# Performance work log

Measured on AMD Instinct MI355X. Metric: run time of the kernel, lower is better.

The kernel has to match this reference:

```python
import jax, jax.numpy as jnp
import numpy as np

HEAD_SIZE = 128
NEG_INF = -1000000000.0

def setup_inputs() -> dict:
    key = jax.random.key(0)
    k1, k2, k3, k4 = jax.random.split(key, 4)
    B, T, C = 8, 2048, 1024
    x = jax.random.normal(k1, (B, T, C), dtype=jnp.float32)
    Wq = jax.random.normal(k2, (C, HEAD_SIZE), dtype=jnp.float32) * (1.0 / np.sqrt(C))
    Wk = jax.random.normal(k3, (C, HEAD_SIZE), dtype=jnp.float32) * (1.0 / np.sqrt(C))
    Wv = jax.random.normal(k4, (C, HEAD_SIZE), dtype=jnp.float32) * (1.0 / np.sqrt(C))
    return {"x": x, "Wq": Wq, "Wk": Wk, "Wv": Wv}

def reference(x, Wq, Wk, Wv):
    # x: [B, T, C]; projections: [B, T, H]
    T = x.shape[1]
    q = jnp.einsum('btc,ch->bth', x, Wq)
    k = jnp.einsum('btc,ch->bth', x, Wk)
    v = jnp.einsum('btc,ch->bth', x, Wv)
    scale = 1.0 / jnp.sqrt(jnp.float32(HEAD_SIZE))
    wei = jnp.einsum('bth,bsh->bts', q, k) * scale  # [B, T, T]
    causal = jnp.tril(jnp.ones((T, T), dtype=bool))
    wei = jnp.where(causal, wei, NEG_INF)
    wei = jax.nn.softmax(wei, axis=-1)
    # dropout is identity (deterministic=True)
    out = jnp.einsum('bts,bsh->bth', wei, v)  # [B, T, H]
    return out
```

## Files before the change

kernel.cpp:

```cpp
#include <hip/hip_runtime.h>
#include <hip/hip_bf16.h>
#include <stdint.h>

#define B_ 8
#define T_ 2048
#define C_ 1024
#define H_ 128
#define BT (B_*T_)
#define SCALE 0.08838834764831845f
#define CH 4
#define SLOTS_PB 140

typedef __attribute__((ext_vector_type(8))) short bf16x8;
typedef __attribute__((ext_vector_type(4))) float f32x4;

__device__ __forceinline__ ushort f2bf(float f) {
  union { float f; uint32_t u; } un; un.f = f;
  return (ushort)((un.u + 0x7fffu + ((un.u >> 16) & 1u)) >> 16);
}
__device__ __forceinline__ float bf2f(ushort h) {
  union { uint32_t u; float f; } un; un.u = ((uint32_t)h) << 16;
  return un.f;
}
__device__ __forceinline__ void gload16(const void* g, void* l) {
  __builtin_amdgcn_global_load_lds(
      (const __attribute__((address_space(1))) void*)g,
      (__attribute__((address_space(3))) void*)l, 16, 0, 0);
}

__global__ __launch_bounds__(256) void wtrans_kernel(
    const float* __restrict__ Wq, const float* __restrict__ Wk,
    const float* __restrict__ Wv, ushort* __restrict__ wt)
{
  const int tt = blockIdx.x * 256 + threadIdx.x;
  const int n = tt >> 6;
  const int k0 = (tt & 63) << 4;
  const float* W = (n < 128) ? Wq : (n < 256 ? Wk : Wv);
  const int h = n & 127;
  ushort tmp[16];
  #pragma unroll
  for (int j = 0; j < 16; ++j)
    tmp[j] = f2bf(W[(size_t)(k0 + j) * H_ + h]);
  *reinterpret_cast<bf16x8*>(&wt[(size_t)n * C_ + k0]) =
      *reinterpret_cast<bf16x8*>(&tmp[0]);
  *reinterpret_cast<bf16x8*>(&wt[(size_t)n * C_ + k0 + 8]) =
      *reinterpret_cast<bf16x8*>(&tmp[8]);
}

__global__ __launch_bounds__(256, 3) void proj_kernel(
    const float* __restrict__ x, const ushort* __restrict__ wt,
    ushort* __restrict__ qh, ushort* __restrict__ kh, ushort* __restrict__ vt)
{
  __shared__ __align__(16) ushort As[64][64];
  __shared__ __align__(16) ushort Bs[128][64];
  const int tid  = threadIdx.x;
  const int lane = tid & 63, wave = tid >> 6;
  const int l15  = lane & 15, l4 = lane >> 4;
  const int o  = (blockIdx.x & 7) * 96 + (blockIdx.x >> 3);
  const int mb = o / 3, nb = o - mb * 3;
  const int m0 = mb * 64, n0 = nb * 128;
  const int wr = wave >> 1, wc = wave & 1;

  f32x4 acc[2][4];
  #pragma unroll
  for (int i = 0; i < 2; ++i)
    #pragma unroll
    for (int j = 0; j < 4; ++j) acc[i][j] = f32x4{0.f, 0.f, 0.f, 0.f};

  for (int k0 = 0; k0 < C_; k0 += 64) {
    __syncthreads();
    #pragma unroll
    for (int j = 0; j < 4; ++j) {
      const int seg = wave * 4 + j;
      const int r = seg * 8 + (lane >> 3);
      const int c8g = (lane & 7) ^ (r & 7);
      gload16(&wt[(size_t)(n0 + r) * C_ + k0 + c8g * 8], &Bs[seg * 8][0]);
    }
    float4 av[4];
    #pragma unroll
    for (int it = 0; it < 4; ++it) {
      const int f4 = it * 256 + tid;
      const int r = f4 >> 4, c4 = f4 & 15;
      av[it] = *reinterpret_cast<const float4*>(
          &x[(size_t)(m0 + r) * C_ + k0 + 4 * c4]);
    }
    #pragma unroll
    for (int it = 0; it < 4; ++it) {
      const int f4 = it * 256 + tid;
      const int r = f4 >> 4, c4 = f4 & 15;
      ushort4 pk;
      pk.x = f2bf(av[it].x); pk.y = f2bf(av[it].y);
      pk.z = f2bf(av[it].z); pk.w = f2bf(av[it].w);
      const int ch = (c4 >> 1) ^ (r & 7);
      *reinterpret_cast<ushort4*>(&As[r][ch * 8 + (c4 & 1) * 4]) = pk;
    }
    __syncthreads();

    bf16x8 a[2][2], b[4][2];
    #pragma unroll
    for (int mi = 0; mi < 2; ++mi)
      #pragma unroll
      for (int kc = 0; kc < 2; ++kc) {
        const int row = wr * 32 + mi * 16 + l15;
        const int ch = (kc * 4 + l4) ^ (row & 7);
        a[mi][kc] = *reinterpret_cast<const bf16x8*>(&As[row][ch * 8]);
      }
    #pragma unroll
    for (int ni = 0; ni < 4; ++ni)
      #pragma unroll
      for (int kc = 0; kc < 2; ++kc) {
        const int row = wc * 64 + ni * 16 + l15;
        const int ch = (kc * 4 + l4) ^ (row & 7);
        b[ni][kc] = *reinterpret_cast<const bf16x8*>(&Bs[row][ch * 8]);
      }

    __builtin_amdgcn_s_setprio(1);
    if (nb != 2) {
      #pragma unroll
      for (int mi = 0; mi < 2; ++mi)
        #pragma unroll
        for (int ni = 0; ni < 4; ++ni)
          #pragma unroll
          for (int kc = 0; kc < 2; ++kc)
            acc[mi][ni] = __builtin_amdgcn_mfma_f32_16x16x32_bf16(
                a[mi][kc], b[ni][kc], acc[mi][ni], 0, 0, 0);
    } else {
      #pragma unroll
      for (int mi = 0; mi < 2; ++mi)
        #pragma unroll
        for (int ni = 0; ni < 4; ++ni)
          #pragma unroll
          for (int kc = 0; kc < 2; ++kc)
            acc[mi][ni] = __builtin_amdgcn_mfma_f32_16x16x32_bf16(
                b[ni][kc], a[mi][kc], acc[mi][ni], 0, 0, 0);
    }
    __builtin_amdgcn_s_setprio(0);
  }

  if (nb != 2) {
    ushort* dst = (nb == 0) ? qh : kh;
    const float mul = (nb == 0) ? SCALE : 1.0f;
    #pragma unroll
    for (int mi = 0; mi < 2; ++mi)
      #pragma unroll
      for (int ni = 0; ni < 4; ++ni)
        #pragma unroll
        for (int reg = 0; reg < 4; ++reg) {
          const int row = m0 + wr * 32 + mi * 16 + l4 * 4 + reg;
          const int col = wc * 64 + ni * 16 + l15;
          dst[(size_t)row * H_ + col] = f2bf(acc[mi][ni][reg] * mul);
        }
  } else {
    #pragma unroll
    for (int mi = 0; mi < 2; ++mi)
      #pragma unroll
      for (int ni = 0; ni < 4; ++ni)
        #pragma unroll
        for (int reg = 0; reg < 4; ++reg) {
          const int h = wc * 64 + ni * 16 + l4 * 4 + reg;
          const int gr = m0 + wr * 32 + mi * 16 + l15;
          const int b = gr >> 11, t = gr & 2047;
          vt[((size_t)b * H_ + h) * T_ + t] = f2bf(acc[mi][ni][reg]);
        }
  }
}

__global__ __launch_bounds__(256) void attn_kernel(
    const ushort* __restrict__ qh, const ushort* __restrict__ kh,
    const ushort* __restrict__ vt, ushort* __restrict__ pO,
    float* __restrict__ pm, float* __restrict__ pl, float* __restrict__ out)
{
  __shared__ __align__(16) ushort Ks[64][128];
  __shared__ __align__(16) ushort Vs[128][64];
  __shared__ __align__(16) ushort Ps[4][16][64];
  const int tid  = threadIdx.x;
  const int lane = tid & 63, wave = tid >> 6;
  const int l15  = lane & 15, l4 = lane >> 4;
  const int o = (blockIdx.x & 7) * 144 + (blockIdx.x >> 3);
  const int b = o / 144;
  const int u = o - b * 144;
  int qi, ci, nchunk, u2 = 0;
  if (u < 4) { qi = u; ci = 0; nchunk = 1; }
  else {
    u2 = u - 4;
    int rem = u2, g = 1;
    while (rem >= 4 * (g + 1)) { rem -= 4 * (g + 1); ++g; }
    nchunk = g + 1;
    qi = 4 * g + rem / nchunk;
    ci = rem - (rem / nchunk) * nchunk;
  }
  const int q0 = qi * 64;
  const int kt0 = ci * CH;
  const int kt1 = min(qi + 1, kt0 + CH);
  const size_t mbase = (size_t)b * T_ + q0;
  const int swz = l15 & 7;

  bf16x8 qa[4];
  {
    const ushort* qrow = &qh[(mbase + wave * 16 + l15) * H_];
    #pragma unroll
    for (int kc = 0; kc < 4; ++kc)
      qa[kc] = *reinterpret_cast<const bf16x8*>(&qrow[kc * 32 + l4 * 8]);
  }

  f32x4 o_[8];
  #pragma unroll
  for (int i = 0; i < 8; ++i) o_[i] = f32x4{0.f, 0.f, 0.f, 0.f};
  float mrow[4] = {-1e9f, -1e9f, -1e9f, -1e9f};
  float lrow[4] = {0.f, 0.f, 0.f, 0.f};

  for (int kt = kt0; kt < kt1; ++kt) {
    const int kv0 = kt * 64;
    __syncthreads();
    #pragma unroll
    for (int j = 0; j < 4; ++j) {
      const int r0 = wave * 16 + j * 4;
      const int r = r0 + (lane >> 4);
      const int c8 = lane & 15;
      const int c8g = (c8 & 8) | ((c8 & 7) ^ (r & 7));
      gload16(&kh[((size_t)b * T_ + kv0 + r) * H_ + c8g * 8], &Ks[r0][0]);
    }
    #pragma unroll
    for (int j = 0; j < 4; ++j) {
      const int r0 = wave * 32 + j * 8;
      const int r = r0 + (lane >> 3);
      const int c8g = (lane & 7) ^ (r & 7);
      gload16(&vt[((size_t)b * H_ + r) * T_ + kv0 + c8g * 8], &Vs[r0][0]);
    }
    __syncthreads();

    f32x4 s[4];
    __builtin_amdgcn_s_setprio(1);
    #pragma unroll
    for (int ct = 0; ct < 4; ++ct) {
      s[ct] = f32x4{0.f, 0.f, 0.f, 0.f};
      #pragma unroll
      for (int kc = 0; kc < 4; ++kc) {
        const int chunk = ((kc * 4 + l4) & 7) ^ swz;
        bf16x8 kb = *reinterpret_cast<const bf16x8*>(
            &Ks[ct * 16 + l15][(((kc * 4 + l4) & 8) | chunk) * 8]);
        s[ct] = __builtin_amdgcn_mfma_f32_16x16x32_bf16(qa[kc], kb, s[ct], 0, 0, 0);
      }
    }
    __builtin_amdgcn_s_setprio(0);

    const bool diag = (kv0 == q0);
    float sv[4][4];
    #pragma unroll
    for (int ct = 0; ct < 4; ++ct)
      #pragma unroll
      for (int reg = 0; reg < 4; ++reg) {
        float v = s[ct][reg];
        if (diag) {
          const int sg = kv0 + ct * 16 + l15;
          const int rg = q0 + wave * 16 + l4 * 4 + reg;
          if (sg > rg) v = -1e9f;
        }
        sv[ct][reg] = v;
      }
    float mnew[4], alpha[4], ls[4];
    #pragma unroll
    for (int reg = 0; reg < 4; ++reg) {
      float m = fmaxf(fmaxf(sv[0][reg], sv[1][reg]), fmaxf(sv[2][reg], sv[3][reg]));
      #pragma unroll
      for (int msk = 1; msk < 16; msk <<= 1) m = fmaxf(m, __shfl_xor(m, msk));
      mnew[reg]  = fmaxf(mrow[reg], m);
      alpha[reg] = __expf(mrow[reg] - mnew[reg]);
      ls[reg] = 0.f;
    }
    #pragma unroll
    for (int ct = 0; ct < 4; ++ct)
      #pragma unroll
      for (int reg = 0; reg < 4; ++reg) {
        const float p = __expf(sv[ct][reg] - mnew[reg]);
        ls[reg] += p;
        const int prow = l4 * 4 + reg;
        Ps[wave][prow][(ct * 16 + l15) ^ ((prow & 7) * 8)] = f2bf(p);
      }
    #pragma unroll
    for (int reg = 0; reg < 4; ++reg) {
      float t = ls[reg];
      #pragma unroll
      for (int msk = 1; msk < 16; msk <<= 1) t += __shfl_xor(t, msk);
      lrow[reg] = lrow[reg] * alpha[reg] + t;
      mrow[reg] = mnew[reg];
    }
    #pragma unroll
    for (int ct = 0; ct < 8; ++ct)
      #pragma unroll
      for (int reg = 0; reg < 4; ++reg) o_[ct][reg] *= alpha[reg];
    bf16x8 pa[2];
    #pragma unroll
    for (int kc = 0; kc < 2; ++kc)
      pa[kc] = *reinterpret_cast<const bf16x8*>(
          &Ps[wave][l15][((kc * 4 + l4) ^ swz) * 8]);
    __builtin_amdgcn_s_setprio(1);
    #pragma unroll
    for (int ct = 0; ct < 8; ++ct) {
      #pragma unroll
      for (int kc = 0; kc < 2; ++kc) {
        bf16x8 vb = *reinterpret_cast<const bf16x8*>(
            &Vs[ct * 16 + l15][((kc * 4 + l4) ^ swz) * 8]);
        o_[ct] = __builtin_amdgcn_mfma_f32_16x16x32_bf16(pa[kc], vb, o_[ct], 0, 0, 0);
      }
    }
    __builtin_amdgcn_s_setprio(0);
  }

  if (nchunk == 1) {
    #pragma unroll
    for (int ct = 0; ct < 8; ++ct)
      #pragma unroll
      for (int reg = 0; reg < 4; ++reg) {
        const size_t row = mbase + wave * 16 + l4 * 4 + reg;
        out[row * H_ + ct * 16 + l15] = o_[ct][reg] / lrow[reg];
      }
  } else {
    const size_t slot = (size_t)b * SLOTS_PB + u2;
    ushort* po = pO + slot * 64 * 128;
    #pragma unroll
    for (int ct = 0; ct < 8; ++ct)
      #pragma unroll
      for (int reg = 0; reg < 4; ++reg) {
        const int row = wave * 16 + l4 * 4 + reg;
        po[(size_t)row * 128 + ct * 16 + l15] = f2bf(o_[ct][reg]);
      }
    #pragma unroll
    for (int reg = 0; reg < 4; ++reg) {
      if (l15 == 0) {
        const int row = wave * 16 + l4 * 4 + reg;
        pm[slot * 64 + row] = mrow[reg];
        pl[slot * 64 + row] = lrow[reg];
      }
    }
  }
}

__global__ __launch_bounds__(256) void combine_kernel(
    const ushort* __restrict__ pO, const float* __restrict__ pm,
    const float* __restrict__ pl, float* __restrict__ out)
{
  const int o = blockIdx.x;
  const int b = o / 28, qi = 4 + o % 28;
  const int G = qi >> 2;
  const int nc = G + 1;
  const int tid = threadIdx.x;
  const int row = tid >> 2, cg = tid & 3;
  const size_t slotbase =
      (size_t)b * SLOTS_PB + 2 * (G - 1) * (G + 2) + (qi & 3) * (G + 1);

  float M = -1e30f;
  for (int ci = 0; ci < nc; ++ci)
    M = fmaxf(M, pm[(slotbase + ci) * 64 + row]);

  float L = 0.f;
  float acc[32];
  #pragma unroll
  for (int j = 0; j < 32; ++j) acc[j] = 0.f;
  for (int ci = 0; ci < nc; ++ci) {
    const float e = __expf(pm[(slotbase + ci) * 64 + row] - M);
    L += pl[(slotbase + ci) * 64 + row] * e;
    const ushort* src = pO + (slotbase + ci) * 8192 + (size_t)row * 128 + cg * 32;
    #pragma unroll
    for (int j4 = 0; j4 < 4; ++j4) {
      bf16x8 v = *reinterpret_cast<const bf16x8*>(&src[j4 * 8]);
      #pragma unroll
      for (int j = 0; j < 8; ++j)
        acc[j4 * 8 + j] += e * bf2f((ushort)v[j]);
    }
  }
  const float inv = 1.f / L;
  float* dst = out + ((size_t)b * T_ + qi * 64 + row) * H_ + cg * 32;
  #pragma unroll
  for (int j4 = 0; j4 < 8; ++j4) {
    float4 w;
    w.x = acc[j4 * 4 + 0] * inv; w.y = acc[j4 * 4 + 1] * inv;
    w.z = acc[j4 * 4 + 2] * inv; w.w = acc[j4 * 4 + 3] * inv;
    *reinterpret_cast<float4*>(&dst[j4 * 4]) = w;
  }
}

extern "C" void kernel_launch(void* const* d_in, const int* in_sizes, int n_in,
                              void* d_out, int out_size, void* d_ws, size_t ws_size,
                              hipStream_t stream) {
  const float* x  = (const float*)d_in[0];
  const float* Wq = (const float*)d_in[1];
  const float* Wk = (const float*)d_in[2];
  const float* Wv = (const float*)d_in[3];
  float* out = (float*)d_out;
  ushort* qh = (ushort*)d_ws;
  ushort* kh = qh + (size_t)BT * H_;
  ushort* vt = kh + (size_t)BT * H_;
  ushort* wt = vt + (size_t)B_ * H_ * T_;
  ushort* pO = wt + (size_t)384 * C_;
  float*  pm = (float*)(pO + (size_t)B_ * SLOTS_PB * 64 * 128);
  float*  pl = pm + (size_t)B_ * SLOTS_PB * 64;
  wtrans_kernel<<<96, 256, 0, stream>>>(Wq, Wk, Wv, wt);
  proj_kernel<<<768, 256, 0, stream>>>(x, wt, qh, kh, vt);
  attn_kernel<<<1152, 256, 0, stream>>>(qh, kh, vt, pO, pm, pl, out);
  combine_kernel<<<224, 256, 0, stream>>>(pO, pm, pl, out);
}
```

Baseline: 79.89 us.

## Prefetch next tile into registers in projection GEMM and attention loops

In the projection GEMM, the next x tile's float4 loads are issued before the current tile is computed, and converted and stored to LDS at the start of the next iteration. In the attention kernel, the direct global-to-LDS K/V loads are replaced by register prefetch of the next K/V tile during compute, written to LDS after a barrier at the end of each iteration. This is meant to hide global memory latency behind MFMA work, at the cost of extra VGPRs (kreg/vreg, av) that may reduce occupancy.

```diff
diff --git a/kernel.cpp b/kernel.cpp
--- a/kernel.cpp
+++ b/kernel.cpp
@@ -67,16 +67,8 @@
     #pragma unroll
     for (int j = 0; j < 4; ++j) acc[i][j] = f32x4{0.f, 0.f, 0.f, 0.f};
 
-  for (int k0 = 0; k0 < C_; k0 += 64) {
-    __syncthreads();
-    #pragma unroll
-    for (int j = 0; j < 4; ++j) {
-      const int seg = wave * 4 + j;
-      const int r = seg * 8 + (lane >> 3);
-      const int c8g = (lane & 7) ^ (r & 7);
-      gload16(&wt[(size_t)(n0 + r) * C_ + k0 + c8g * 8], &Bs[seg * 8][0]);
-    }
-    float4 av[4];
+  float4 av[4];
+  auto a_issue = [&](int k0) {
     #pragma unroll
     for (int it = 0; it < 4; ++it) {
       const int f4 = it * 256 + tid;
@@ -84,6 +76,8 @@
       av[it] = *reinterpret_cast<const float4*>(
           &x[(size_t)(m0 + r) * C_ + k0 + 4 * c4]);
     }
+  };
+  auto a_write = [&]() {
     #pragma unroll
     for (int it = 0; it < 4; ++it) {
       const int f4 = it * 256 + tid;
@@ -94,6 +88,21 @@
       const int ch = (c4 >> 1) ^ (r & 7);
       *reinterpret_cast<ushort4*>(&As[r][ch * 8 + (c4 & 1) * 4]) = pk;
     }
+  };
+
+  a_issue(0);
+  for (int t = 0; t < 16; ++t) {
+    const int k0 = t * 64;
+    __syncthreads();
+    #pragma unroll
+    for (int j = 0; j < 4; ++j) {
+      const int seg = wave * 4 + j;
+      const int r = seg * 8 + (lane >> 3);
+      const int c8g = (lane & 7) ^ (r & 7);
+      gload16(&wt[(size_t)(n0 + r) * C_ + k0 + c8g * 8], &Bs[seg * 8][0]);
+    }
+    a_write();
+    if (t < 15) a_issue(k0 + 64);
     __syncthreads();
 
     bf16x8 a[2][2], b[4][2];
@@ -203,31 +212,53 @@
       qa[kc] = *reinterpret_cast<const bf16x8*>(&qrow[kc * 32 + l4 * 8]);
   }
 
+  bf16x8 kreg[4], vreg[4];
+  auto kv_issue = [&](int kv0) {
+    #pragma unroll
+    for (int j = 0; j < 4; ++j) {
+      const int i = j * 256 + tid;
+      const int r = i >> 4, c8 = i & 15;
+      kreg[j] = *reinterpret_cast<const bf16x8*>(
+          &kh[((size_t)b * T_ + kv0 + r) * H_ + c8 * 8]);
+    }
+    #pragma unroll
+    for (int j = 0; j < 4; ++j) {
+      const int i = j * 256 + tid;
+      const int r = i >> 3, c8 = i & 7;
+      vreg[j] = *reinterpret_cast<const bf16x8*>(
+          &vt[((size_t)b * H_ + r) * T_ + kv0 + c8 * 8]);
+    }
+  };
+  auto kv_write = [&]() {
+    #pragma unroll
+    for (int j = 0; j < 4; ++j) {
+      const int i = j * 256 + tid;
+      const int r = i >> 4, c8 = i & 15;
+      const int c8s = (c8 & 7) ^ (r & 7);
+      *reinterpret_cast<bf16x8*>(&Ks[r][((c8 & 8) | c8s) * 8]) = kreg[j];
+    }
+    #pragma unroll
+    for (int j = 0; j < 4; ++j) {
+      const int i = j * 256 + tid;
+      const int r = i >> 3, c8 = i & 7;
+      const int c8s = c8 ^ (r & 7);
+      *reinterpret_cast<bf16x8*>(&Vs[r][c8s * 8]) = vreg[j];
+    }
+  };
+
   f32x4 o_[8];
   #pragma unroll
   for (int i = 0; i < 8; ++i) o_[i] = f32x4{0.f, 0.f, 0.f, 0.f};
   float mrow[4] = {-1e9f, -1e9f, -1e9f, -1e9f};
   float lrow[4] = {0.f, 0.f, 0.f, 0.f};
 
+  kv_issue(kt0 * 64);
+  kv_write();
+
   for (int kt = kt0; kt < kt1; ++kt) {
     const int kv0 = kt * 64;
     __syncthreads();
-    #pragma unroll
-    for (int j = 0; j < 4; ++j) {
-      const int r0 = wave * 16 + j * 4;
-      const int r = r0 + (lane >> 4);
-      const int c8 = lane & 15;
-      const int c8g = (c8 & 8) | ((c8 & 7) ^ (r & 7));
-      gload16(&kh[((size_t)b * T_ + kv0 + r) * H_ + c8g * 8], &Ks[r0][0]);
-    }
-    #pragma unroll
-    for (int j = 0; j < 4; ++j) {
-      const int r0 = wave * 32 + j * 8;
-      const int r = r0 + (lane >> 3);
-      const int c8g = (lane & 7) ^ (r & 7);
-      gload16(&vt[((size_t)b * H_ + r) * T_ + kv0 + c8g * 8], &Vs[r0][0]);
-    }
-    __syncthreads();
+    if (kt + 1 < kt1) kv_issue((kt + 1) * 64);
 
     f32x4 s[4];
     __builtin_amdgcn_s_setprio(1);
@@ -305,6 +336,9 @@
       }
     }
     __builtin_amdgcn_s_setprio(0);
+
+    __syncthreads();
+    if (kt + 1 < kt1) kv_write();
   }
 
   if (nchunk == 1) {
```

New measurement: 80.56 us. Within noise of the previous version (+0.8%).

## Double-buffer projection GEMM and load weights directly into registers

Applied to the files above, without the earlier changes.

Rewrites the projection kernel's K loop as a software pipeline. The A tile is double-buffered in LDS, and the next step's x and weight loads are issued before the current step's MFMAs. Weight fragments now go from global memory straight into registers, so the Bs shared tile and its LDS round trip are gone. This should hide global-load latency and leave one barrier per step, but it raises register pressure and makes weight reads uncoalesced, which may conflict with the occupancy target of 3 set in the launch bounds.

```diff
diff --git a/kernel.cpp b/kernel.cpp
--- a/kernel.cpp
+++ b/kernel.cpp
@@ -51,8 +51,8 @@
     const float* __restrict__ x, const ushort* __restrict__ wt,
     ushort* __restrict__ qh, ushort* __restrict__ kh, ushort* __restrict__ vt)
 {
-  __shared__ __align__(16) ushort As[64][64];
-  __shared__ __align__(16) ushort Bs[128][64];
+  __shared__ __align__(16) ushort As0[64][64];
+  __shared__ __align__(16) ushort As1[64][64];
   const int tid  = threadIdx.x;
   const int lane = tid & 63, wave = tid >> 6;
   const int l15  = lane & 15, l4 = lane >> 4;
@@ -67,74 +67,89 @@
     #pragma unroll
     for (int j = 0; j < 4; ++j) acc[i][j] = f32x4{0.f, 0.f, 0.f, 0.f};
 
-  for (int k0 = 0; k0 < C_; k0 += 64) {
-    __syncthreads();
-    #pragma unroll
-    for (int j = 0; j < 4; ++j) {
-      const int seg = wave * 4 + j;
-      const int r = seg * 8 + (lane >> 3);
-      const int c8g = (lane & 7) ^ (r & 7);
-      gload16(&wt[(size_t)(n0 + r) * C_ + k0 + c8g * 8], &Bs[seg * 8][0]);
-    }
-    float4 av[4];
-    #pragma unroll
-    for (int it = 0; it < 4; ++it) {
-      const int f4 = it * 256 + tid;
-      const int r = f4 >> 4, c4 = f4 & 15;
-      av[it] = *reinterpret_cast<const float4*>(
-          &x[(size_t)(m0 + r) * C_ + k0 + 4 * c4]);
-    }
-    #pragma unroll
-    for (int it = 0; it < 4; ++it) {
-      const int f4 = it * 256 + tid;
-      const int r = f4 >> 4, c4 = f4 & 15;
-      ushort4 pk;
-      pk.x = f2bf(av[it].x); pk.y = f2bf(av[it].y);
-      pk.z = f2bf(av[it].z); pk.w = f2bf(av[it].w);
-      const int ch = (c4 >> 1) ^ (r & 7);
-      *reinterpret_cast<ushort4*>(&As[r][ch * 8 + (c4 & 1) * 4]) = pk;
-    }
-    __syncthreads();
-
-    bf16x8 a[2][2], b[4][2];
-    #pragma unroll
-    for (int mi = 0; mi < 2; ++mi)
-      #pragma unroll
-      for (int kc = 0; kc < 2; ++kc) {
-        const int row = wr * 32 + mi * 16 + l15;
-        const int ch = (kc * 4 + l4) ^ (row & 7);
-        a[mi][kc] = *reinterpret_cast<const bf16x8*>(&As[row][ch * 8]);
-      }
-    #pragma unroll
-    for (int ni = 0; ni < 4; ++ni)
-      #pragma unroll
-      for (int kc = 0; kc < 2; ++kc) {
-        const int row = wc * 64 + ni * 16 + l15;
-        const int ch = (kc * 4 + l4) ^ (row & 7);
-        b[ni][kc] = *reinterpret_cast<const bf16x8*>(&Bs[row][ch * 8]);
-      }
-
-    __builtin_amdgcn_s_setprio(1);
-    if (nb != 2) {
-      #pragma unroll
-      for (int mi = 0; mi < 2; ++mi)
-        #pragma unroll
-        for (int ni = 0; ni < 4; ++ni)
-          #pragma unroll
-          for (int kc = 0; kc < 2; ++kc)
-            acc[mi][ni] = __builtin_amdgcn_mfma_f32_16x16x32_bf16(
-                a[mi][kc], b[ni][kc], acc[mi][ni], 0, 0, 0);
-    } else {
-      #pragma unroll
-      for (int mi = 0; mi < 2; ++mi)
-        #pragma unroll
-        for (int ni = 0; ni < 4; ++ni)
-          #pragma unroll
-          for (int kc = 0; kc < 2; ++kc)
-            acc[mi][ni] = __builtin_amdgcn_mfma_f32_16x16x32_bf16(
-                b[ni][kc], a[mi][kc], acc[mi][ni], 0, 0, 0);
-    }
-    __builtin_amdgcn_s_setprio(0);
+  float4 av[4];
+  bf16x8 b0[4][2], b1[4][2];
+
+#define X_ISSUE(K0) do {                                                   \
+    _Pragma("unroll")                                                      \
+    for (int it = 0; it < 4; ++it) {                                       \
+      const int f4 = it * 256 + tid;                                       \
+      const int r = f4 >> 4, c4 = f4 & 15;                                 \
+      av[it] = *reinterpret_cast<const float4*>(                           \
+          &x[(size_t)(m0 + r) * C_ + (K0) + 4 * c4]);                      \
+    } } while (0)
+
+#define B_ISSUE(K0, BB) do {                                               \
+    _Pragma("unroll")                                                      \
+    for (int ni = 0; ni < 4; ++ni)                                         \
+      _Pragma("unroll")                                                    \
+      for (int kc = 0; kc < 2; ++kc)                                       \
+        BB[ni][kc] = *reinterpret_cast<const bf16x8*>(                     \
+            &wt[(size_t)(n0 + wc * 64 + ni * 16 + l15) * C_ +              \
+                (K0) + kc * 32 + l4 * 8]);                                 \
+    } while (0)
+
+#define A_WRITE(DST) do {                                                  \
+    _Pragma("unroll")                                                      \
+    for (int it = 0; it < 4; ++it) {                                       \
+      const int f4 = it * 256 + tid;                                       \
+      const int r = f4 >> 4, c4 = f4 & 15;                                 \
+      ushort4 pk;                                                          \
+      pk.x = f2bf(av[it].x); pk.y = f2bf(av[it].y);                        \
+      pk.z = f2bf(av[it].z); pk.w = f2bf(av[it].w);                        \
+      const int ch = (c4 >> 1) ^ (r & 7);                                  \
+      *reinterpret_cast<ushort4*>(&DST[r][ch * 8 + (c4 & 1) * 4]) = pk;    \
+    } } while (0)
+
+#define LDS_FENCE() do {                                                   \
+    asm volatile("s_waitcnt lgkmcnt(0)" ::: "memory");                     \
+    __builtin_amdgcn_sched_barrier(0);                                     \
+    __builtin_amdgcn_s_barrier();                                          \
+  } while (0)
+
+#define PROJ_STEP(T, CURB, NXTB, BCUR, BNXT) do {                          \
+    bf16x8 a[2][2];                                                        \
+    _Pragma("unroll")                                                      \
+    for (int mi = 0; mi < 2; ++mi)                                         \
+      _Pragma("unroll")                                                    \
+      for (int kc = 0; kc < 2; ++kc) {                                     \
+        const int row = wr * 32 + mi * 16 + l15;                           \
+        const int ch = (kc * 4 + l4) ^ (row & 7);                          \
+        a[mi][kc] = *reinterpret_cast<const bf16x8*>(&CURB[row][ch * 8]);  \
+      }                                                                    \
+    if ((T) < 15) { X_ISSUE(((T) + 1) * 64); B_ISSUE(((T) + 1) * 64, BNXT); } \
+    __builtin_amdgcn_s_setprio(1);                                         \
+    if (nb != 2) {                                                         \
+      _Pragma("unroll")                                                    \
+      for (int mi = 0; mi < 2; ++mi)                                       \
+        _Pragma("unroll")                                                  \
+        for (int ni = 0; ni < 4; ++ni)                                     \
+          _Pragma("unroll")                                                \
+          for (int kc = 0; kc < 2; ++kc)                                   \
+            acc[mi][ni] = __builtin_amdgcn_mfma_f32_16x16x32_bf16(         \
+                a[mi][kc], BCUR[ni][kc], acc[mi][ni], 0, 0, 0);            \
+    } else {                                                               \
+      _Pragma("unroll")                                                    \
+      for (int mi = 0; mi < 2; ++mi)                                       \
+        _Pragma("unroll")                                                  \
+        for (int ni = 0; ni < 4; ++ni)                                     \
+          _Pragma("unroll")                                                \
+          for (int kc = 0; kc < 2; ++kc)                                   \
+            acc[mi][ni] = __builtin_amdgcn_mfma_f32_16x16x32_bf16(         \
+                BCUR[ni][kc], a[mi][kc], acc[mi][ni], 0, 0, 0);            \
+    }                                                                      \
+    __builtin_amdgcn_s_setprio(0);                                         \
+    if ((T) < 15) { A_WRITE(NXTB); LDS_FENCE(); }                          \
+  } while (0)
+
+  X_ISSUE(0);
+  B_ISSUE(0, b0);
+  A_WRITE(As0);
+  LDS_FENCE();
+
+  for (int tt = 0; tt < 8; ++tt) {
+    PROJ_STEP(2 * tt,     As0, As1, b0, b1);
+    PROJ_STEP(2 * tt + 1, As1, As0, b1, b0);
   }
 
   if (nb != 2) {
```

Measured after the change: 162.0 us. 2.03x slower.
